# Optimization experiments

Hardware: AMD Instinct MI355X
Metric: run time of the kernel (lower is better)

Reference implementation:

```python
import jax, jax.numpy as jnp
import numpy as np

N_ATOMS = 100000
N_BONDS = 400000
ATOM_FDIM = 133
BOND_FDIM = 147
HIDDEN = 300
DEPTH = 3


def setup_inputs() -> dict:
    key = jax.random.key(0)
    ks = jax.random.split(key, 10)
    f_atoms = jax.random.normal(ks[0], (N_ATOMS, ATOM_FDIM), dtype=jnp.float32)
    f_bonds = jax.random.normal(ks[1], (N_BONDS, BOND_FDIM), dtype=jnp.float32)
    b2a = jax.random.randint(ks[2], (N_BONDS,), 0, N_ATOMS)
    b2revb = jax.random.randint(ks[3], (N_BONDS,), 0, N_BONDS)
    s_i = 1.0 / np.sqrt(BOND_FDIM)
    s_h = 1.0 / np.sqrt(HIDDEN)
    s_o = 1.0 / np.sqrt(ATOM_FDIM + HIDDEN)
    Wi_w = jax.random.uniform(ks[4], (HIDDEN, BOND_FDIM), jnp.float32, -s_i, s_i)
    Wi_b = jax.random.uniform(ks[5], (HIDDEN,), jnp.float32, -s_i, s_i)
    Wh_w = jax.random.uniform(ks[6], (HIDDEN, HIDDEN), jnp.float32, -s_h, s_h)
    Wh_b = jax.random.uniform(ks[7], (HIDDEN,), jnp.float32, -s_h, s_h)
    Wo_w = jax.random.uniform(ks[8], (HIDDEN, ATOM_FDIM + HIDDEN), jnp.float32, -s_o, s_o)
    Wo_b = jax.random.uniform(ks[9], (HIDDEN,), jnp.float32, -s_o, s_o)
    return {"f_atoms": f_atoms, "f_bonds": f_bonds, "b2a": b2a, "b2revb": b2revb,
            "Wi_w": Wi_w, "Wi_b": Wi_b, "Wh_w": Wh_w, "Wh_b": Wh_b,
            "Wo_w": Wo_w, "Wo_b": Wo_b}


def reference(f_atoms, f_bonds, b2a, b2revb, Wi_w, Wi_b, Wh_w, Wh_b, Wo_w, Wo_b):
    n_atoms = f_atoms.shape[0]
    # initial bond messages: [n_bonds, hidden]
    H_bonds = jax.nn.relu(f_bonds @ Wi_w.T + Wi_b)
    dest = b2a[b2revb]  # destination atom of each directed bond
    for _ in range(DEPTH - 1):
        # scatter-add bond messages onto destination atoms
        sum_msgs = jax.ops.segment_sum(H_bonds, dest, num_segments=n_atoms)
        # gather back to bonds from source atoms, subtract reverse-bond message
        msgs = sum_msgs[b2a] - H_bonds[b2revb]
        H_bonds = jax.nn.relu(H_bonds + msgs @ Wh_w.T + Wh_b)
    sum_msgs = jax.ops.segment_sum(H_bonds, dest, num_segments=n_atoms)
    H_atoms = jax.nn.relu(jnp.concatenate([f_atoms, sum_msgs], axis=1) @ Wo_w.T + Wo_b)
    return (H_atoms, H_bonds)
```

## Files before the change

kernel.cpp:

```cpp
#include <hip/hip_runtime.h>
#include <hip/hip_bf16.h>

#define NB 400000
#define NA 100000
#define AFD 133
#define BFD 147
#define HID 300
#define NP  320
#define NT  98

typedef short short8 __attribute__((ext_vector_type(8)));
typedef float f32x4 __attribute__((ext_vector_type(4)));

__device__ __forceinline__ ushort f2b(float f) {
    union { float f; unsigned u; } v; v.f = f;
    unsigned r = v.u + 0x7fffu + ((v.u >> 16) & 1u);
    return (ushort)(r >> 16);
}
__device__ __forceinline__ float b2f(ushort u) {
    union { unsigned u; float f; } v; v.u = ((unsigned)u) << 16;
    return v.f;
}

#define GLDS(gp, lp) __builtin_amdgcn_global_load_lds( \
    (const __attribute__((address_space(1))) void*)(gp), \
    (__attribute__((address_space(3))) void*)(lp), 16, 0, 0)


__global__ void pad_w_k(const float* __restrict__ W, ushort* __restrict__ Wp,
                        int N, int K, int Kp) {
    int idx = blockIdx.x * 256 + threadIdx.x;
    if (idx >= NP * Kp) return;
    int n = idx / Kp, k = idx - n * Kp;
    int t = k >> 5, kk = k & 31;
    int g = kk >> 3, s = kk & 7;
    int gp = g ^ ((n >> 1) & 3);
    ushort v = (n < N && k < K) ? f2b(W[n * K + k]) : (ushort)0;
    Wp[(size_t)t * 10240 + n * 32 + gp * 8 + s] = v;
}

__global__ void pad_bias_k(const float* __restrict__ bh, float* __restrict__ bhp) {
    int i = blockIdx.x * 256 + threadIdx.x;
    if (i < NP) bhp[i] = (i < HID) ? bh[i] : 0.f;
}

__global__ void dest_k(const int* __restrict__ b2a, const int* __restrict__ b2revb,
                       int* __restrict__ dest) {
    int b = blockIdx.x * 256 + threadIdx.x;
    if (b < NB) dest[b] = b2a[b2revb[b]];
}

__global__ void count_k(const int* __restrict__ dest, int* __restrict__ cnt) {
    int b = blockIdx.x * 256 + threadIdx.x;
    if (b < NB) atomicAdd(&cnt[dest[b]], 1);
}

__global__ void scanA_k(const int* __restrict__ cnt, int* __restrict__ tsum) {
    __shared__ int sm[256];
    const int tid = threadIdx.x;
    int base = blockIdx.x * 1024 + tid * 4;
    int s = 0;
#pragma unroll
    for (int j = 0; j < 4; ++j) { int i = base + j; if (i < NA) s += cnt[i]; }
    sm[tid] = s; __syncthreads();
    for (int o = 128; o > 0; o >>= 1) {
        if (tid < o) sm[tid] += sm[tid + o];
        __syncthreads();
    }
    if (tid == 0) tsum[blockIdx.x] = sm[0];
}

__global__ void scanB_k(const int* __restrict__ tsum, int* __restrict__ toff,
                        int* __restrict__ rs) {
    if (threadIdx.x == 0) {
        int run = 0;
        for (int t = 0; t < NT; ++t) { toff[t] = run; run += tsum[t]; }
        rs[NA] = run;
    }
}

__global__ void scanC_k(const int* __restrict__ cnt, const int* __restrict__ toff,
                        int* __restrict__ rs) {
    __shared__ int sm[256];
    const int tid = threadIdx.x;
    int base = blockIdx.x * 1024 + tid * 4;
    int v[4]; int s = 0;
#pragma unroll
    for (int j = 0; j < 4; ++j) {
        v[j] = (base + j < NA) ? cnt[base + j] : 0;
        s += v[j];
    }
    sm[tid] = s; __syncthreads();
    for (int o = 1; o < 256; o <<= 1) {
        int x = (tid >= o) ? sm[tid - o] : 0;
        __syncthreads();
        sm[tid] += x;
        __syncthreads();
    }
    int acc = sm[tid] - s + toff[blockIdx.x];
#pragma unroll
    for (int j = 0; j < 4; ++j) {
        if (base + j < NA) rs[base + j] = acc;
        acc += v[j];
    }
}

__global__ void scatter_k(const int* __restrict__ dest, const int* __restrict__ rs,
                          int* __restrict__ cur, int* __restrict__ bl) {
    int b = blockIdx.x * 256 + threadIdx.x;
    if (b >= NB) return;
    int a = dest[b];
    int pos = rs[a] + atomicAdd(&cur[a], 1);
    bl[pos] = b;
}

template<int MODE>
__global__ __launch_bounds__(512) void gemm_k(
    const float* __restrict__ F1, const ushort* __restrict__ SHb,
    const ushort* __restrict__ W, const float* __restrict__ bias,
    ushort* __restrict__ Cb, float* __restrict__ Cf, int M)
{
    constexpr int KP = (MODE == 0) ? 192 : 448;
    constexpr int TILES = KP / 32;
    static_assert(KP % 64 == 0 && TILES % 2 == 0, "XOR swizzle needs 128B rows, even tiles");
    __shared__ char smem[(128 * KP + 2 * 10240) * 2];
    ushort (*Bs)[10240] = (ushort (*)[10240])(smem + 128 * KP * 2);

    const int tid = threadIdx.x;
    const int w = tid >> 6, lane = tid & 63;
    const int wr = w >> 2, wc = w & 3;
    const int g = lane >> 4, lr = lane & 15;
    const int m0 = blockIdx.x * 128;

    {
        const int row = tid >> 2, q = tid & 3;
        int grow = m0 + row;
        if (MODE == 2 && grow >= M) grow = M - 1;
        const int axw = (row & 7) << 4;
        char* abase = smem + (size_t)row * (KP * 2);
#pragma unroll
        for (int t = 0; t < TILES; ++t) {
            const int k0 = t * 32 + q * 8;
            ushort o[8];
            if (MODE == 0) {
                const float* src = F1 + (size_t)grow * BFD;
#pragma unroll
                for (int s = 0; s < 8; ++s)
                    o[s] = (k0 + s < BFD) ? f2b(src[k0 + s]) : (ushort)0;
            } else {
#pragma unroll
                for (int s = 0; s < 8; ++s) {
                    int k = k0 + s;
                    o[s] = (k < AFD) ? f2b(F1[(size_t)grow * AFD + k])
                                     : SHb[(size_t)grow * NP + (k - AFD)];
                }
            }
            ushort* dst = (ushort*)(abase + ((t * 64 + q * 16) ^ axw));
            *(ushort4*)dst       = make_ushort4(o[0], o[1], o[2], o[3]);
            *(ushort4*)(dst + 4) = make_ushort4(o[4], o[5], o[6], o[7]);
        }
    }

    auto stageB = [&](int t, int buf) {
        const ushort* wt = W + (size_t)t * 10240;
        ushort* bs = &Bs[buf][0];
        GLDS(wt + (size_t)w * 512 + lane * 8,        bs + w * 512);
        GLDS(wt + (size_t)(w + 8) * 512 + lane * 8,  bs + (w + 8) * 512);
        if (w < 4)
            GLDS(wt + (size_t)(w + 16) * 512 + lane * 8, bs + (w + 16) * 512);
    };

    f32x4 acc[4][5];
#pragma unroll
    for (int mi = 0; mi < 4; ++mi)
#pragma unroll
        for (int ni = 0; ni < 5; ++ni) acc[mi][ni] = (f32x4){0.f, 0.f, 0.f, 0.f};

    stageB(0, 0);
    __syncthreads();

    const int raxw = (lr & 7) << 4;
    const int bswz = (lr >> 1) & 3;
    for (int t = 0; t < TILES; ++t) {
        if (t + 1 < TILES) stageB(t + 1, (t + 1) & 1);
        const ushort* bs = &Bs[t & 1][0];
        short8 af[4];
#pragma unroll
        for (int mi = 0; mi < 4; ++mi) {
            const int r = wr * 64 + mi * 16 + lr;
            af[mi] = *(const short8*)(smem + (size_t)r * (KP * 2)
                                      + ((t * 64 + g * 16) ^ raxw));
        }
#pragma unroll
        for (int ni = 0; ni < 5; ++ni) {
            const int c = wc * 80 + ni * 16 + lr;
            short8 bf = *(const short8*)&bs[c * 32 + ((g ^ bswz) << 3)];
#pragma unroll
            for (int mi = 0; mi < 4; ++mi)
                acc[mi][ni] = __builtin_amdgcn_mfma_f32_16x16x32_bf16(af[mi], bf, acc[mi][ni], 0, 0, 0);
        }
        __syncthreads();
    }

    if (MODE == 0) {
        float* EP = (float*)smem;
        for (int ph = 0; ph < 4; ++ph) {
            __syncthreads();
            if (wc == ph) {
#pragma unroll
                for (int mi = 0; mi < 4; ++mi)
#pragma unroll
                    for (int ni = 0; ni < 5; ++ni) {
                        const int ec = ni * 16 + lr;
#pragma unroll
                        for (int r = 0; r < 4; ++r)
                            EP[(wr * 64 + mi * 16 + g * 4 + r) * 84 + ec] = acc[mi][ni][r];
                    }
            }
            __syncthreads();
            for (int it2 = tid; it2 < 2560; it2 += 512) {
                const int row = it2 / 20, cc = (it2 - row * 20) * 4;
                const int grow = m0 + row;
                const int col = ph * 80 + cc;
                float4 a = *(const float4*)&EP[row * 84 + cc];
                float4 bb = (col < HID) ? *(const float4*)&bias[col]
                                        : make_float4(0.f, 0.f, 0.f, 0.f);
                *(ushort4*)&Cb[(size_t)grow * NP + col] =
                    make_ushort4(f2b(fmaxf(a.x + bb.x, 0.f)), f2b(fmaxf(a.y + bb.y, 0.f)),
                                 f2b(fmaxf(a.z + bb.z, 0.f)), f2b(fmaxf(a.w + bb.w, 0.f)));
            }
        }
    } else {
#pragma unroll
        for (int ni = 0; ni < 5; ++ni) {
            const int col = wc * 80 + ni * 16 + lr;
            const float bv = (col < HID) ? bias[col] : 0.f;
#pragma unroll
            for (int mi = 0; mi < 4; ++mi) {
                const int row0 = m0 + wr * 64 + mi * 16 + g * 4;
#pragma unroll
                for (int r = 0; r < 4; ++r) {
                    const int row = row0 + r;
                    float v = fmaxf(acc[mi][ni][r] + bv, 0.f);
                    if (col < HID && row < M) Cf[(size_t)row * HID + col] = v;
                }
            }
        }
    }
}

__global__ __launch_bounds__(512) void gemm_h_k(
    const ushort* __restrict__ Hb, const ushort* __restrict__ W,
    ushort* __restrict__ Y)
{
    __shared__ char smem[57344];
    ushort (*As)[4][128][8] = (ushort (*)[4][128][8])smem;
    ushort (*Bs)[10240] = (ushort (*)[10240])(smem + 16384);
    const int tid = threadIdx.x;
    const int w = tid >> 6, lane = tid & 63;
    const int wr = w >> 2, wc = w & 3;
    const int g = lane >> 4, lr = lane & 15;
    const int m0 = blockIdx.x * 128;

    const int q = w >> 1, r0 = (w & 1) * 64;
    const ushort* aglob = Hb + (size_t)(m0 + r0 + lane) * NP + q * 8;

    f32x4 acc[4][5];
#pragma unroll
    for (int mi = 0; mi < 4; ++mi)
#pragma unroll
        for (int ni = 0; ni < 5; ++ni) acc[mi][ni] = (f32x4){0.f, 0.f, 0.f, 0.f};

    auto stageA = [&](int t, int buf) { GLDS(aglob + t * 32, &As[buf][q][r0][0]); };
    auto stageB = [&](int t, int buf) {
        const ushort* wt = W + (size_t)t * 10240;
        ushort* bs = &Bs[buf][0];
        GLDS(wt + (size_t)w * 512 + lane * 8,        bs + w * 512);
        GLDS(wt + (size_t)(w + 8) * 512 + lane * 8,  bs + (w + 8) * 512);
        if (w < 4)
            GLDS(wt + (size_t)(w + 16) * 512 + lane * 8, bs + (w + 16) * 512);
    };

    stageA(0, 0); stageB(0, 0);
    __syncthreads();

    const int bswz = (lr >> 1) & 3;
    for (int t = 0; t < 10; ++t) {
        if (t < 9) { stageA(t + 1, (t + 1) & 1); stageB(t + 1, (t + 1) & 1); }
        const int buf = t & 1;
        short8 af[4];
#pragma unroll
        for (int mi = 0; mi < 4; ++mi)
            af[mi] = *(const short8*)&As[buf][g][wr * 64 + mi * 16 + lr][0];
#pragma unroll
        for (int ni = 0; ni < 5; ++ni) {
            const int c = wc * 80 + ni * 16 + lr;
            short8 bf = *(const short8*)&Bs[buf][c * 32 + ((g ^ bswz) << 3)];
#pragma unroll
            for (int mi = 0; mi < 4; ++mi)
                acc[mi][ni] = __builtin_amdgcn_mfma_f32_16x16x32_bf16(af[mi], bf, acc[mi][ni], 0, 0, 0);
        }
        __syncthreads();
    }

    float* EP = (float*)smem;
    for (int ph = 0; ph < 4; ++ph) {
        __syncthreads();
        if (wc == ph) {
#pragma unroll
            for (int mi = 0; mi < 4; ++mi)
#pragma unroll
                for (int ni = 0; ni < 5; ++ni) {
                    const int ec = ni * 16 + lr;
#pragma unroll
                    for (int r = 0; r < 4; ++r)
                        EP[(wr * 64 + mi * 16 + g * 4 + r) * 84 + ec] = acc[mi][ni][r];
                }
        }
        __syncthreads();
        for (int it2 = tid; it2 < 2560; it2 += 512) {
            const int row = it2 / 20, cc = (it2 - row * 20) * 4;
            const int col = ph * 80 + cc;
            float4 a = *(const float4*)&EP[row * 84 + cc];
            *(ushort4*)&Y[(size_t)(m0 + row) * NP + col] =
                make_ushort4(f2b(a.x), f2b(a.y), f2b(a.z), f2b(a.w));
        }
    }
}

__global__ void seg_sum_bf16_k(const ushort* __restrict__ H, const int* __restrict__ rs,
                               const int* __restrict__ bl, ushort* __restrict__ SH) {
    int idx = blockIdx.x * 256 + threadIdx.x;
    if (idx >= NA * 40) return;
    int a = idx / 40, c = (idx - a * 40) * 8;
    int s0 = rs[a], s1 = rs[a + 1];
    float acc[8] = {0.f, 0.f, 0.f, 0.f, 0.f, 0.f, 0.f, 0.f};
    for (int j = s0; j < s1; ++j) {
        const ushort* p = &H[(size_t)bl[j] * NP + c];
        ushort4 u0 = *(const ushort4*)p, u1 = *(const ushort4*)(p + 4);
        acc[0] += b2f(u0.x); acc[1] += b2f(u0.y);
        acc[2] += b2f(u0.z); acc[3] += b2f(u0.w);
        acc[4] += b2f(u1.x); acc[5] += b2f(u1.y);
        acc[6] += b2f(u1.z); acc[7] += b2f(u1.w);
    }
    ushort* dst = &SH[(size_t)a * NP + c];
    *(ushort4*)dst       = make_ushort4(f2b(acc[0]), f2b(acc[1]), f2b(acc[2]), f2b(acc[3]));
    *(ushort4*)(dst + 4) = make_ushort4(f2b(acc[4]), f2b(acc[5]), f2b(acc[6]), f2b(acc[7]));
}

template<bool OUTF>
__global__ void update_k(ushort* __restrict__ Hb, const ushort* __restrict__ SY,
                         const ushort* __restrict__ Y,
                         const int* __restrict__ b2a, const int* __restrict__ b2revb,
                         const float* __restrict__ bhp, float* __restrict__ Hbonds) {
    int idx = blockIdx.x * 256 + threadIdx.x;
    if (idx >= NB * 40) return;
    int b = idx / 40, c = (idx - b * 40) * 8;
    int sa = b2a[b], rb = b2revb[b];
    ushort* hp = &Hb[(size_t)b * NP + c];
    const ushort* sp = &SY[(size_t)sa * NP + c];
    const ushort* yp = &Y[(size_t)rb * NP + c];
    ushort4 h0 = *(const ushort4*)hp,       h1 = *(const ushort4*)(hp + 4);
    ushort4 s0 = *(const ushort4*)sp,       s1 = *(const ushort4*)(sp + 4);
    ushort4 y0 = *(const ushort4*)yp,       y1 = *(const ushort4*)(yp + 4);
    float4 bl0 = *(const float4*)&bhp[c], bl1 = *(const float4*)&bhp[c + 4];
    float v[8];
    v[0] = fmaxf(b2f(h0.x) + b2f(s0.x) - b2f(y0.x) + bl0.x, 0.f);
    v[1] = fmaxf(b2f(h0.y) + b2f(s0.y) - b2f(y0.y) + bl0.y, 0.f);
    v[2] = fmaxf(b2f(h0.z) + b2f(s0.z) - b2f(y0.z) + bl0.z, 0.f);
    v[3] = fmaxf(b2f(h0.w) + b2f(s0.w) - b2f(y0.w) + bl0.w, 0.f);
    v[4] = fmaxf(b2f(h1.x) + b2f(s1.x) - b2f(y1.x) + bl1.x, 0.f);
    v[5] = fmaxf(b2f(h1.y) + b2f(s1.y) - b2f(y1.y) + bl1.y, 0.f);
    v[6] = fmaxf(b2f(h1.z) + b2f(s1.z) - b2f(y1.z) + bl1.z, 0.f);
    v[7] = fmaxf(b2f(h1.w) + b2f(s1.w) - b2f(y1.w) + bl1.w, 0.f);
    *(ushort4*)hp       = make_ushort4(f2b(v[0]), f2b(v[1]), f2b(v[2]), f2b(v[3]));
    *(ushort4*)(hp + 4) = make_ushort4(f2b(v[4]), f2b(v[5]), f2b(v[6]), f2b(v[7]));
    if (OUTF && c < HID) {
        float* op = &Hbonds[(size_t)b * HID + c];
        *(float4*)op = make_float4(v[0], v[1], v[2], v[3]);
        if (c + 4 < HID) *(float4*)(op + 4) = make_float4(v[4], v[5], v[6], v[7]);
    }
}

extern "C" void kernel_launch(void* const* d_in, const int* in_sizes, int n_in,
                              void* d_out, int out_size, void* d_ws, size_t ws_size,
                              hipStream_t stream) {
    const float* f_atoms = (const float*)d_in[0];
    const float* f_bonds = (const float*)d_in[1];
    const int*   b2a     = (const int*)d_in[2];
    const int*   b2revb  = (const int*)d_in[3];
    const float* Wi_w    = (const float*)d_in[4];
    const float* Wi_b    = (const float*)d_in[5];
    const float* Wh_w    = (const float*)d_in[6];
    const float* Wh_b    = (const float*)d_in[7];
    const float* Wo_w    = (const float*)d_in[8];
    const float* Wo_b    = (const float*)d_in[9];
    float* out = (float*)d_out;

    char* ws = (char*)d_ws;
    ushort* Hb   = (ushort*)ws;            ws += (size_t)NB * NP * 2;
    ushort* Y    = (ushort*)ws;            ws += (size_t)NB * NP * 2;
    ushort* SY   = (ushort*)ws;            ws += (size_t)NA * NP * 2;
    int*    dest = (int*)ws;               ws += (size_t)NB * 4;
    ushort* Wp0  = (ushort*)ws;            ws += (size_t)6  * 10240 * 2;
    ushort* Wp1  = (ushort*)ws;            ws += (size_t)10 * 10240 * 2;
    ushort* Wp2  = (ushort*)ws;            ws += (size_t)14 * 10240 * 2;
    float*  bhp  = (float*)ws;             ws += (size_t)NP * 4;
    int*    cnt  = (int*)ws;               ws += (size_t)NA * 4;
    int*    cur  = (int*)ws;               ws += (size_t)NA * 4;
    int*    rs   = (int*)ws;               ws += (size_t)(NA + 1) * 4;
    int*    bl   = (int*)ws;               ws += (size_t)NB * 4;
    int*    tsum = (int*)ws;               ws += 128 * 4;
    int*    toff = (int*)ws;               ws += 128 * 4;
    float* Hatoms = out;
    float* Hbonds = out + (size_t)NA * HID;

    pad_w_k<<<(NP * 192 + 255) / 256, 256, 0, stream>>>(Wi_w, Wp0, HID, BFD, 192);
    pad_w_k<<<(NP * NP  + 255) / 256, 256, 0, stream>>>(Wh_w, Wp1, HID, HID, NP);
    pad_w_k<<<(NP * 448 + 255) / 256, 256, 0, stream>>>(Wo_w, Wp2, HID, AFD + HID, 448);
    pad_bias_k<<<2, 256, 0, stream>>>(Wh_b, bhp);
    dest_k<<<(NB + 255) / 256, 256, 0, stream>>>(b2a, b2revb, dest);
    hipMemsetAsync(cnt, 0, (size_t)NA * 4, stream);
    hipMemsetAsync(cur, 0, (size_t)NA * 4, stream);
    count_k<<<(NB + 255) / 256, 256, 0, stream>>>(dest, cnt);
    scanA_k<<<NT, 256, 0, stream>>>(cnt, tsum);
    scanB_k<<<1, 64, 0, stream>>>(tsum, toff, rs);
    scanC_k<<<NT, 256, 0, stream>>>(cnt, toff, rs);
    scatter_k<<<(NB + 255) / 256, 256, 0, stream>>>(dest, rs, cur, bl);

    gemm_k<0><<<NB / 128, 512, 0, stream>>>(
        f_bonds, nullptr, Wp0, Wi_b, Hb, nullptr, NB);

    for (int it = 0; it < 2; ++it) {
        gemm_h_k<<<NB / 128, 512, 0, stream>>>(Hb, Wp1, Y);
        seg_sum_bf16_k<<<(NA * 40 + 255) / 256, 256, 0, stream>>>(Y, rs, bl, SY);
        if (it == 0)
            update_k<false><<<(NB * 40 + 255) / 256, 256, 0, stream>>>(
                Hb, SY, Y, b2a, b2revb, bhp, nullptr);
        else
            update_k<true><<<(NB * 40 + 255) / 256, 256, 0, stream>>>(
                Hb, SY, Y, b2a, b2revb, bhp, Hbonds);
    }

    seg_sum_bf16_k<<<(NA * 40 + 255) / 256, 256, 0, stream>>>(Hb, rs, bl, SY);
    gemm_k<2><<<(NA + 127) / 128, 512, 0, stream>>>(
        f_atoms, SY, Wp2, Wo_b, nullptr, Hatoms, NA);
}
```

Measured before the change: 1.536 ms.

## Merge prep kernels and load GEMM A operand directly into registers

The three weight-padding kernels and the bias pad are folded into one launch. The dest and count kernels are fused, and the two memsets become one since cnt and cur are adjacent. The hidden GEMM no longer stages A tiles through LDS via global_load_lds. Each lane now loads its A fragments straight from global memory into registers with a one-tile register prefetch, which cuts LDS use and one set of LDS reads but makes global loads uncoalesced and puts their latency on the critical path.

```diff
diff --git a/kernel.cpp b/kernel.cpp
--- a/kernel.cpp
+++ b/kernel.cpp
@@ -27,10 +27,9 @@
     (__attribute__((address_space(3))) void*)(lp), 16, 0, 0)
 
 
-__global__ void pad_w_k(const float* __restrict__ W, ushort* __restrict__ Wp,
-                        int N, int K, int Kp) {
-    int idx = blockIdx.x * 256 + threadIdx.x;
-    if (idx >= NP * Kp) return;
+__device__ __forceinline__ void pad_one(const float* __restrict__ W,
+                                        ushort* __restrict__ Wp,
+                                        int idx, int N, int K, int Kp) {
     int n = idx / Kp, k = idx - n * Kp;
     int t = k >> 5, kk = k & 31;
     int g = kk >> 3, s = kk & 7;
@@ -39,20 +38,28 @@
     Wp[(size_t)t * 10240 + n * 32 + gp * 8 + s] = v;
 }
 
-__global__ void pad_bias_k(const float* __restrict__ bh, float* __restrict__ bhp) {
-    int i = blockIdx.x * 256 + threadIdx.x;
-    if (i < NP) bhp[i] = (i < HID) ? bh[i] : 0.f;
-}
-
-__global__ void dest_k(const int* __restrict__ b2a, const int* __restrict__ b2revb,
-                       int* __restrict__ dest) {
+__global__ void prep_w_k(const float* __restrict__ Wi, const float* __restrict__ Wh,
+                         const float* __restrict__ Wo, const float* __restrict__ bh,
+                         ushort* __restrict__ Wp0, ushort* __restrict__ Wp1,
+                         ushort* __restrict__ Wp2, float* __restrict__ bhp) {
+    int idx = blockIdx.x * 256 + threadIdx.x;
+    const int n0 = NP * 192, n1 = NP * 320, n2 = NP * 448;
+    if (idx < n0) { pad_one(Wi, Wp0, idx, HID, BFD, 192); return; }
+    idx -= n0;
+    if (idx < n1) { pad_one(Wh, Wp1, idx, HID, HID, 320); return; }
+    idx -= n1;
+    if (idx < n2) { pad_one(Wo, Wp2, idx, HID, AFD + HID, 448); return; }
+    idx -= n2;
+    if (idx < NP) bhp[idx] = (idx < HID) ? bh[idx] : 0.f;
+}
+
+__global__ void dest_count_k(const int* __restrict__ b2a, const int* __restrict__ b2revb,
+                             int* __restrict__ dest, int* __restrict__ cnt) {
     int b = blockIdx.x * 256 + threadIdx.x;
-    if (b < NB) dest[b] = b2a[b2revb[b]];
-}
-
-__global__ void count_k(const int* __restrict__ dest, int* __restrict__ cnt) {
-    int b = blockIdx.x * 256 + threadIdx.x;
-    if (b < NB) atomicAdd(&cnt[dest[b]], 1);
+    if (b >= NB) return;
+    int d = b2a[b2revb[b]];
+    dest[b] = d;
+    atomicAdd(&cnt[d], 1);
 }
 
 __global__ void scanA_k(const int* __restrict__ cnt, int* __restrict__ tsum) {
@@ -123,7 +130,7 @@
     constexpr int KP = (MODE == 0) ? 192 : 448;
     constexpr int TILES = KP / 32;
     static_assert(KP % 64 == 0 && TILES % 2 == 0, "XOR swizzle needs 128B rows, even tiles");
-    __shared__ char smem[(128 * KP + 2 * 10240) * 2];
+    __shared__ __align__(16) char smem[(128 * KP + 2 * 10240) * 2];
     ushort (*Bs)[10240] = (ushort (*)[10240])(smem + 128 * KP * 2);
 
     const int tid = threadIdx.x;
@@ -253,25 +260,14 @@
     const ushort* __restrict__ Hb, const ushort* __restrict__ W,
     ushort* __restrict__ Y)
 {
-    __shared__ char smem[57344];
-    ushort (*As)[4][128][8] = (ushort (*)[4][128][8])smem;
-    ushort (*Bs)[10240] = (ushort (*)[10240])(smem + 16384);
+    __shared__ __align__(16) char smem[43008];
+    ushort (*Bs)[10240] = (ushort (*)[10240])smem;
     const int tid = threadIdx.x;
     const int w = tid >> 6, lane = tid & 63;
     const int wr = w >> 2, wc = w & 3;
     const int g = lane >> 4, lr = lane & 15;
     const int m0 = blockIdx.x * 128;
 
-    const int q = w >> 1, r0 = (w & 1) * 64;
-    const ushort* aglob = Hb + (size_t)(m0 + r0 + lane) * NP + q * 8;
-
-    f32x4 acc[4][5];
-#pragma unroll
-    for (int mi = 0; mi < 4; ++mi)
-#pragma unroll
-        for (int ni = 0; ni < 5; ++ni) acc[mi][ni] = (f32x4){0.f, 0.f, 0.f, 0.f};
-
-    auto stageA = [&](int t, int buf) { GLDS(aglob + t * 32, &As[buf][q][r0][0]); };
     auto stageB = [&](int t, int buf) {
         const ushort* wt = W + (size_t)t * 10240;
         ushort* bs = &Bs[buf][0];
@@ -281,26 +277,46 @@
             GLDS(wt + (size_t)(w + 16) * 512 + lane * 8, bs + (w + 16) * 512);
     };
 
-    stageA(0, 0); stageB(0, 0);
+    f32x4 acc[4][5];
+#pragma unroll
+    for (int mi = 0; mi < 4; ++mi)
+#pragma unroll
+        for (int ni = 0; ni < 5; ++ni) acc[mi][ni] = (f32x4){0.f, 0.f, 0.f, 0.f};
+
+    const ushort* arow[4];
+#pragma unroll
+    for (int mi = 0; mi < 4; ++mi)
+        arow[mi] = Hb + (size_t)(m0 + wr * 64 + mi * 16 + lr) * NP + g * 8;
+
+    stageB(0, 0);
+    short8 afc[4];
+#pragma unroll
+    for (int mi = 0; mi < 4; ++mi) afc[mi] = *(const short8*)arow[mi];
     __syncthreads();
 
     const int bswz = (lr >> 1) & 3;
     for (int t = 0; t < 10; ++t) {
-        if (t < 9) { stageA(t + 1, (t + 1) & 1); stageB(t + 1, (t + 1) & 1); }
-        const int buf = t & 1;
-        short8 af[4];
-#pragma unroll
-        for (int mi = 0; mi < 4; ++mi)
-            af[mi] = *(const short8*)&As[buf][g][wr * 64 + mi * 16 + lr][0];
+        if (t < 9) stageB(t + 1, (t + 1) & 1);
+        short8 afn[4];
+        if (t < 9) {
+#pragma unroll
+            for (int mi = 0; mi < 4; ++mi)
+                afn[mi] = *(const short8*)(arow[mi] + (t + 1) * 32);
+        }
+        const ushort* bs = &Bs[t & 1][0];
 #pragma unroll
         for (int ni = 0; ni < 5; ++ni) {
             const int c = wc * 80 + ni * 16 + lr;
-            short8 bf = *(const short8*)&Bs[buf][c * 32 + ((g ^ bswz) << 3)];
+            short8 bf = *(const short8*)&bs[c * 32 + ((g ^ bswz) << 3)];
 #pragma unroll
             for (int mi = 0; mi < 4; ++mi)
-                acc[mi][ni] = __builtin_amdgcn_mfma_f32_16x16x32_bf16(af[mi], bf, acc[mi][ni], 0, 0, 0);
-        }
-        __syncthreads();
+                acc[mi][ni] = __builtin_amdgcn_mfma_f32_16x16x32_bf16(afc[mi], bf, acc[mi][ni], 0, 0, 0);
+        }
+        __syncthreads();
+        if (t < 9) {
+#pragma unroll
+            for (int mi = 0; mi < 4; ++mi) afc[mi] = afn[mi];
+        }
     }
 
     float* EP = (float*)smem;
@@ -415,14 +431,11 @@
     float* Hatoms = out;
     float* Hbonds = out + (size_t)NA * HID;
 
-    pad_w_k<<<(NP * 192 + 255) / 256, 256, 0, stream>>>(Wi_w, Wp0, HID, BFD, 192);
-    pad_w_k<<<(NP * NP  + 255) / 256, 256, 0, stream>>>(Wh_w, Wp1, HID, HID, NP);
-    pad_w_k<<<(NP * 448 + 255) / 256, 256, 0, stream>>>(Wo_w, Wp2, HID, AFD + HID, 448);
-    pad_bias_k<<<2, 256, 0, stream>>>(Wh_b, bhp);
-    dest_k<<<(NB + 255) / 256, 256, 0, stream>>>(b2a, b2revb, dest);
-    hipMemsetAsync(cnt, 0, (size_t)NA * 4, stream);
-    hipMemsetAsync(cur, 0, (size_t)NA * 4, stream);
-    count_k<<<(NB + 255) / 256, 256, 0, stream>>>(dest, cnt);
+    const int prep_n = NP * 192 + NP * 320 + NP * 448 + NP;
+    prep_w_k<<<(prep_n + 255) / 256, 256, 0, stream>>>(
+        Wi_w, Wh_w, Wo_w, Wh_b, Wp0, Wp1, Wp2, bhp);
+    hipMemsetAsync(cnt, 0, (size_t)2 * NA * 4, stream);
+    dest_count_k<<<(NB + 255) / 256, 256, 0, stream>>>(b2a, b2revb, dest, cnt);
     scanA_k<<<NT, 256, 0, stream>>>(cnt, tsum);
     scanB_k<<<1, 64, 0, stream>>>(tsum, toff, rs);
     scanC_k<<<NT, 256, 0, stream>>>(cnt, toff, rs);
```

Measured after the change: 1.645 ms. +7.1%, slower.
